# Kernel optimization log

Hardware: AMD Instinct MI355X
Metric: run time of the kernel (lower is better)

## Reference

```python
import jax, jax.numpy as jnp
import numpy as np

D_IN = 1024
D_OUT = 1024
N_HEADS = 16
HEAD_DIM = D_IN // N_HEADS      # 64
HEAD_DIM_V = D_OUT // N_HEADS   # 64


def setup_inputs() -> dict:
    key = jax.random.key(0)
    ks = jax.random.split(key, 7)
    s = 0.02
    x = jax.random.normal(ks[0], (4, 2048, D_IN), dtype=jnp.float32)
    Wq = jax.random.normal(ks[1], (D_IN, D_IN), dtype=jnp.float32) * s
    bq = jnp.zeros((D_IN,), dtype=jnp.float32)
    Wk = jax.random.normal(ks[2], (D_IN, D_IN), dtype=jnp.float32) * s
    bk = jnp.zeros((D_IN,), dtype=jnp.float32)
    Wv = jax.random.normal(ks[3], (D_IN, D_OUT), dtype=jnp.float32) * s
    bv = jnp.zeros((D_OUT,), dtype=jnp.float32)
    return {"x": x, "Wq": Wq, "bq": bq, "Wk": Wk, "bk": bk, "Wv": Wv, "bv": bv}


def reference(x, Wq, bq, Wk, bk, Wv, bv):
    B, S, _ = x.shape
    scale = jnp.sqrt(jnp.asarray(HEAD_DIM, dtype=jnp.float32))
    # projections -> [B, S, H, Dh] -> [B, H, S, Dh]
    q = (x @ Wq + bq).reshape(B, S, N_HEADS, HEAD_DIM).transpose(0, 2, 1, 3)
    k = (x @ Wk + bk).reshape(B, S, N_HEADS, HEAD_DIM).transpose(0, 2, 1, 3)
    v = (x @ Wv + bv).reshape(B, S, N_HEADS, HEAD_DIM_V).transpose(0, 2, 1, 3)
    # [B, H, S, S] attention scores (naive full materialization, as in source)
    scores = jnp.einsum("bhsd,bhtd->bhst", q, k) / scale
    weights = jax.nn.softmax(scores, axis=-1)
    out = jnp.einsum("bhst,bhtd->bhsd", weights, v)
    # [B, H, S, Dv] -> [B, S, H*Dv]  (out_projection NOT applied in source forward)
    return out.transpose(0, 2, 1, 3).reshape(B, S, N_HEADS * HEAD_DIM_V)
```

## Files before the change

### kernel.cpp

```cpp
#include <hip/hip_runtime.h>

#define B_  4
#define S_  2048
#define D_  1024
#define H_  16
#define DH_ 64
#define M_  (B_ * S_)

typedef __attribute__((ext_vector_type(8))) short short8;
typedef __attribute__((ext_vector_type(4))) float floatx4;

__device__ __forceinline__ float bf2f(unsigned short u) {
    union { unsigned int i; float f; } v; v.i = ((unsigned int)u) << 16; return v.f;
}
__device__ __forceinline__ unsigned short f2bf(float f) {
    union { float f; unsigned int i; } v; v.f = f;
    unsigned int r = v.i + 0x7fffu + ((v.i >> 16) & 1u);
    return (unsigned short)(r >> 16);
}
__device__ __forceinline__ unsigned int pk_trunc(float a, float b) {
#if __has_builtin(__builtin_amdgcn_perm)
    return __builtin_amdgcn_perm(__float_as_uint(b), __float_as_uint(a), 0x07060302u);
#else
    return (__float_as_uint(a) >> 16) | (__float_as_uint(b) & 0xffff0000u);
#endif
}

#if __has_builtin(__builtin_amdgcn_exp2f)
#define EXP2(x) __builtin_amdgcn_exp2f(x)
#else
#define EXP2(x) __expf(0.6931471805599453f * (x))
#endif

typedef const __attribute__((address_space(1))) unsigned int* gas_ptr;
typedef __attribute__((address_space(3))) unsigned int* las_ptr;
__device__ __forceinline__ void async_cp16(const void* g, void* l) {
    __builtin_amdgcn_global_load_lds((gas_ptr)g, (las_ptr)l, 16, 0, 0);
}

__global__ __launch_bounds__(256) void cast_x_kernel(
    const float* __restrict__ x, unsigned short* __restrict__ Ax)
{
    int i4 = blockIdx.x * 256 + threadIdx.x;
    float4 v = reinterpret_cast<const float4*>(x)[i4];
    ushort4 o;
    o.x = f2bf(v.x); o.y = f2bf(v.y); o.z = f2bf(v.z); o.w = f2bf(v.w);
    reinterpret_cast<ushort4*>(Ax)[i4] = o;
}

__global__ __launch_bounds__(256) void cast_w_T_kernel(
    const float* __restrict__ W0, const float* __restrict__ W1,
    const float* __restrict__ W2,
    unsigned short* __restrict__ T0, unsigned short* __restrict__ T1,
    unsigned short* __restrict__ T2)
{
    const float* W = blockIdx.z == 0 ? W0 : (blockIdx.z == 1 ? W1 : W2);
    unsigned short* Wt = blockIdx.z == 0 ? T0 : (blockIdx.z == 1 ? T1 : T2);

    __shared__ unsigned short T[64][72];
    const int t = threadIdx.x;
    const int k0 = blockIdx.x * 64, n0 = blockIdx.y * 64;

    #pragma unroll
    for (int p = 0; p < 4; ++p) {
        int kr = p * 16 + (t >> 4);
        int nc = (t & 15) * 4;
        float4 v = *reinterpret_cast<const float4*>(W + (size_t)(k0 + kr) * D_ + n0 + nc);
        T[nc + 0][kr] = f2bf(v.x);
        T[nc + 1][kr] = f2bf(v.y);
        T[nc + 2][kr] = f2bf(v.z);
        T[nc + 3][kr] = f2bf(v.w);
    }
    __syncthreads();

    const int nl = t >> 2, kc = (t & 3) * 16;
    size_t base = (size_t)(n0 + nl) * D_ + k0 + kc;
    *reinterpret_cast<short8*>(Wt + base)     = *reinterpret_cast<const short8*>(&T[nl][kc]);
    *reinterpret_cast<short8*>(Wt + base + 8) = *reinterpret_cast<const short8*>(&T[nl][kc + 8]);
}

__global__ __launch_bounds__(256) void gemm_qkv_mfma(
    const unsigned short* __restrict__ Ax,
    const unsigned short* __restrict__ Wtq,
    const unsigned short* __restrict__ Wtk,
    const unsigned short* __restrict__ Wtv,
    const float* __restrict__ bq, const float* __restrict__ bk,
    const float* __restrict__ bv,
    unsigned short* __restrict__ Q, unsigned short* __restrict__ K,
    unsigned short* __restrict__ Vtg)
{
    __shared__ unsigned short As[128 * 64];
    __shared__ unsigned short Bs[128 * 64];

    const int tid = threadIdx.x;
    const int lane = tid & 63;
    const int w = tid >> 6;
    const int wm = (w >> 1) * 64, wn = (w & 1) * 64;
    const int l15 = lane & 15, quad = lane >> 4;

    const int hw   = blockIdx.x;
    const int xcd  = hw & 7;
    const int slot = hw >> 3;
    const int gcol = slot >> 3;
    const int mi   = slot & 7;
    const int m0   = (xcd * 8 + mi) * 128;
    const int n0   = (gcol & 7) * 128;
    const int mat  = gcol >> 3;

    const unsigned short* Wt = mat == 0 ? Wtq : (mat == 1 ? Wtk : Wtv);
    const float* bias        = mat == 0 ? bq  : (mat == 1 ? bk  : bv);

    const int arow = tid >> 3;
    const int acol = (tid & 7) * 8;

    floatx4 acc[4][4] = {};

    for (int kb = 0; kb < 16; ++kb) {
        int cb = kb * 64;
        __syncthreads();
        #pragma unroll
        for (int r = 0; r < 4; ++r) {
            async_cp16(Ax + (size_t)(m0 + r * 32 + arow) * D_ + cb + acol,
                       As + (r * 32 + arow) * 64 + acol);
            async_cp16(Wt + (size_t)(n0 + r * 32 + arow) * D_ + cb + acol,
                       Bs + (r * 32 + arow) * 64 + acol);
        }
        __syncthreads();

        #pragma unroll
        for (int kk = 0; kk < 2; ++kk) {
            short8 af[4], bf[4];
            #pragma unroll
            for (int i = 0; i < 4; ++i)
                af[i] = *reinterpret_cast<const short8*>(As + (wm + i * 16 + l15) * 64 + kk * 32 + quad * 8);
            #pragma unroll
            for (int j = 0; j < 4; ++j)
                bf[j] = *reinterpret_cast<const short8*>(Bs + (wn + j * 16 + l15) * 64 + kk * 32 + quad * 8);
            #pragma unroll
            for (int i = 0; i < 4; ++i)
                #pragma unroll
                for (int j = 0; j < 4; ++j)
                    acc[i][j] = __builtin_amdgcn_mfma_f32_16x16x32_bf16(af[i], bf[j], acc[i][j], 0, 0, 0);
        }
    }

    float bb[4];
    #pragma unroll
    for (int j = 0; j < 4; ++j) bb[j] = bias[n0 + wn + j * 16 + l15];

    if (mat == 2) {
        const int b = m0 >> 11;
        #pragma unroll
        for (int i = 0; i < 4; ++i) {
            int srow = (m0 & 2047) + wm + i * 16 + quad * 4;
            #pragma unroll
            for (int j = 0; j < 4; ++j) {
                int col = n0 + wn + j * 16 + l15;
                ushort4 o;
                o.x = f2bf(acc[i][j][0] + bb[j]);
                o.y = f2bf(acc[i][j][1] + bb[j]);
                o.z = f2bf(acc[i][j][2] + bb[j]);
                o.w = f2bf(acc[i][j][3] + bb[j]);
                *reinterpret_cast<ushort4*>(Vtg + (size_t)(b * 1024 + col) * S_ + srow) = o;
            }
        }
    } else {
        unsigned short* C = (mat == 0) ? Q : K;
        const float sc = (mat == 0) ? 0.18033688011112042f : 1.0f;
        #pragma unroll
        for (int i = 0; i < 4; ++i)
            #pragma unroll
            for (int r = 0; r < 4; ++r) {
                int row = m0 + wm + i * 16 + quad * 4 + r;
                #pragma unroll
                for (int j = 0; j < 4; ++j)
                    C[(size_t)row * D_ + n0 + wn + j * 16 + l15] = f2bf((acc[i][j][r] + bb[j]) * sc);
            }
    }
}

#define KT_   64
#define PITCH 72

__global__ __launch_bounds__(256, 4) void attn_mfma(
    const unsigned short* __restrict__ Qg,
    const unsigned short* __restrict__ Kg,
    const unsigned short* __restrict__ Vtg,
    float* __restrict__ out)
{
    __shared__ unsigned short Ks[KT_ * PITCH];
    __shared__ unsigned short Vt[DH_ * PITCH];

    const int tid  = threadIdx.x;
    const int wq   = tid >> 6;
    const int lane = tid & 63;
    const int l15  = lane & 15;
    const int quad = lane >> 4;

    const int id  = blockIdx.x;
    const int bh  = (id & 7) * 8 + ((id >> 3) & 7);
    const int qt  = id >> 6;
    const int b   = bh >> 4;
    const int colbase = (bh & 15) * DH_;
    const int rowQ0 = b * S_ + qt * 128;

    short8 qf[2][2];
    #pragma unroll
    for (int g = 0; g < 2; ++g) {
        int qrow = rowQ0 + wq * 32 + g * 16 + l15;
        qf[g][0] = *reinterpret_cast<const short8*>(Qg + (size_t)qrow * D_ + colbase + quad * 8);
        qf[g][1] = *reinterpret_cast<const short8*>(Qg + (size_t)qrow * D_ + colbase + 32 + quad * 8);
    }

    short8 vones;
    #pragma unroll
    for (int i = 0; i < 8; ++i) vones[i] = (short)0x3F80;

    floatx4 Oacc[2][4] = {};
    floatx4 Lacc[2] = {};

    const int srow = tid >> 3;
    const int sc8  = (tid & 7) * 8;
    const int vc  = sc8 >> 4;
    const int vqk = (sc8 >> 2) & 3;
    const int vk0 = ((vc & 1) << 2) + ((vc >> 1) << 5) + (vqk << 3);

    const unsigned short* Kbase = Kg + (size_t)(b * S_) * D_ + colbase;
    const unsigned short* Vbase = Vtg + (size_t)(bh * 64) * S_;

    short8 kpre[2], vpre[2];
    #pragma unroll
    for (int p = 0; p < 2; ++p) {
        kpre[p] = *reinterpret_cast<const short8*>(Kbase + (size_t)(p * 32 + srow) * D_ + sc8);
        vpre[p] = *reinterpret_cast<const short8*>(Vbase + (size_t)(p * 32 + srow) * S_ + sc8);
    }

    for (int kt = 0; kt < S_ / KT_; ++kt) {
        __syncthreads();
        #pragma unroll
        for (int p = 0; p < 2; ++p) {
            *reinterpret_cast<short8*>(&Ks[(p * 32 + srow) * PITCH + sc8]) = kpre[p];
            uint4 u = __builtin_bit_cast(uint4, vpre[p]);
            uint2 lo, hi;
            lo.x = u.x; lo.y = u.y; hi.x = u.z; hi.y = u.w;
            *reinterpret_cast<uint2*>(&Vt[(p * 32 + srow) * PITCH + vk0])     = lo;
            *reinterpret_cast<uint2*>(&Vt[(p * 32 + srow) * PITCH + vk0 + 8]) = hi;
        }
        if (kt + 1 < S_ / KT_) {
            int off = (kt + 1) * KT_;
            #pragma unroll
            for (int p = 0; p < 2; ++p) {
                kpre[p] = *reinterpret_cast<const short8*>(Kbase + (size_t)(off + p * 32 + srow) * D_ + sc8);
                vpre[p] = *reinterpret_cast<const short8*>(Vbase + (size_t)(p * 32 + srow) * S_ + off + sc8);
            }
        }
        __syncthreads();

        #pragma unroll
        for (int half = 0; half < 2; ++half) {
            floatx4 s_[2][2];
            #pragma unroll
            for (int ci = 0; ci < 2; ++ci) {
                int c = half * 2 + ci;
                short8 kf0 = *reinterpret_cast<const short8*>(&Ks[(c * 16 + l15) * PITCH + quad * 8]);
                short8 kf1 = *reinterpret_cast<const short8*>(&Ks[(c * 16 + l15) * PITCH + 32 + quad * 8]);
                #pragma unroll
                for (int g = 0; g < 2; ++g) {
                    floatx4 a = {0.f, 0.f, 0.f, 0.f};
                    a = __builtin_amdgcn_mfma_f32_16x16x32_bf16(kf0, qf[g][0], a, 0, 0, 0);
                    a = __builtin_amdgcn_mfma_f32_16x16x32_bf16(kf1, qf[g][1], a, 0, 0, 0);
                    s_[g][ci] = a;
                }
            }
            short8 pa[2];
            #pragma unroll
            for (int g = 0; g < 2; ++g) {
                float p00 = EXP2(s_[g][0][0]), p01 = EXP2(s_[g][0][1]);
                float p02 = EXP2(s_[g][0][2]), p03 = EXP2(s_[g][0][3]);
                float p10 = EXP2(s_[g][1][0]), p11 = EXP2(s_[g][1][1]);
                float p12 = EXP2(s_[g][1][2]), p13 = EXP2(s_[g][1][3]);
                uint4 pu;
                pu.x = pk_trunc(p00, p01);
                pu.y = pk_trunc(p02, p03);
                pu.z = pk_trunc(p10, p11);
                pu.w = pk_trunc(p12, p13);
                pa[g] = __builtin_bit_cast(short8, pu);
            }
            #pragma unroll
            for (int g = 0; g < 2; ++g)
                Lacc[g] = __builtin_amdgcn_mfma_f32_16x16x32_bf16(pa[g], vones, Lacc[g], 0, 0, 0);
            #pragma unroll
            for (int d = 0; d < 4; ++d) {
                short8 vf = *reinterpret_cast<const short8*>(
                    &Vt[(d * 16 + l15) * PITCH + half * 32 + quad * 8]);
                #pragma unroll
                for (int g = 0; g < 2; ++g)
                    Oacc[g][d] = __builtin_amdgcn_mfma_f32_16x16x32_bf16(pa[g], vf, Oacc[g][d], 0, 0, 0);
            }
        }
    }

    #pragma unroll
    for (int g = 0; g < 2; ++g) {
        int orow = rowQ0 + wq * 32 + g * 16 + quad * 4;
        #pragma unroll
        for (int r = 0; r < 4; ++r) {
            float inv = 1.f / Lacc[g][r];
            #pragma unroll
            for (int d = 0; d < 4; ++d)
                out[(size_t)(orow + r) * D_ + colbase + d * 16 + l15] = Oacc[g][d][r] * inv;
        }
    }
}

extern "C" void kernel_launch(void* const* d_in, const int* in_sizes, int n_in,
                              void* d_out, int out_size, void* d_ws, size_t ws_size,
                              hipStream_t stream) {
    const float* x  = (const float*)d_in[0];
    const float* Wq = (const float*)d_in[1];
    const float* bq = (const float*)d_in[2];
    const float* Wk = (const float*)d_in[3];
    const float* bk = (const float*)d_in[4];
    const float* Wv = (const float*)d_in[5];
    const float* bv = (const float*)d_in[6];
    float* out = (float*)d_out;

    unsigned short* Q   = (unsigned short*)d_ws;
    unsigned short* K   = Q + (size_t)M_ * D_;
    unsigned short* Vtg = K + (size_t)M_ * D_;
    unsigned short* Ax  = Vtg + (size_t)M_ * D_;
    unsigned short* Wtq = Ax + (size_t)M_ * D_;
    unsigned short* Wtk = Wtq + (size_t)D_ * D_;
    unsigned short* Wtv = Wtk + (size_t)D_ * D_;

    cast_x_kernel<<<M_ * D_ / 4 / 256, 256, 0, stream>>>(x, Ax);
    dim3 gw(16, 16, 3);
    cast_w_T_kernel<<<gw, 256, 0, stream>>>(Wq, Wk, Wv, Wtq, Wtk, Wtv);

    gemm_qkv_mfma<<<1536, 256, 0, stream>>>(Ax, Wtq, Wtk, Wtv, bq, bk, bv, Q, K, Vtg);

    attn_mfma<<<1024, 256, 0, stream>>>(Q, K, Vtg, out);
}
```

Baseline: 246.0 us.

## Rewrite QKV GEMM as 256x256-tile, 8-wave, multi-stage async-pipelined kernel

Replaces the 128x128 single-buffered QKV projection GEMM with a 256x256 tile per 512-thread block. It uses a three-stage async global-to-LDS pipeline with explicit vmcnt waits, an XOR-swizzled LDS layout, and interleaved barriers with setprio around the MFMA bursts. The goal is to hide global load latency, cut LDS bank conflicts and raise operand reuse per tile. In exchange it uses 128 KB of LDS, which allows one block per CU. The grid shrinks to 384 blocks, so the GEMM may suffer tail and occupancy effects.

```diff
diff --git a/kernel.cpp b/kernel.cpp
--- a/kernel.cpp
+++ b/kernel.cpp
@@ -37,6 +37,9 @@
 __device__ __forceinline__ void async_cp16(const void* g, void* l) {
     __builtin_amdgcn_global_load_lds((gas_ptr)g, (las_ptr)l, 16, 0, 0);
 }
+
+#define VMC4 asm volatile("s_waitcnt vmcnt(4)" ::: "memory")
+#define VMC0 asm volatile("s_waitcnt vmcnt(0)" ::: "memory")
 
 __global__ __launch_bounds__(256) void cast_x_kernel(
     const float* __restrict__ x, unsigned short* __restrict__ Ax)
@@ -79,7 +82,7 @@
     *reinterpret_cast<short8*>(Wt + base + 8) = *reinterpret_cast<const short8*>(&T[nl][kc + 8]);
 }
 
-__global__ __launch_bounds__(256) void gemm_qkv_mfma(
+__global__ __launch_bounds__(512) void gemm_qkv_mfma(
     const unsigned short* __restrict__ Ax,
     const unsigned short* __restrict__ Wtq,
     const unsigned short* __restrict__ Wtk,
@@ -89,92 +92,127 @@
     unsigned short* __restrict__ Q, unsigned short* __restrict__ K,
     unsigned short* __restrict__ Vtg)
 {
-    __shared__ unsigned short As[128 * 64];
-    __shared__ unsigned short Bs[128 * 64];
-
-    const int tid = threadIdx.x;
+    __shared__ unsigned short lds[65536];
+
+    const int tid  = threadIdx.x;
     const int lane = tid & 63;
-    const int w = tid >> 6;
-    const int wm = (w >> 1) * 64, wn = (w & 1) * 64;
-    const int l15 = lane & 15, quad = lane >> 4;
-
-    const int hw   = blockIdx.x;
-    const int xcd  = hw & 7;
-    const int slot = hw >> 3;
-    const int gcol = slot >> 3;
-    const int mi   = slot & 7;
-    const int m0   = (xcd * 8 + mi) * 128;
-    const int n0   = (gcol & 7) * 128;
-    const int mat  = gcol >> 3;
-
-    const unsigned short* Wt = mat == 0 ? Wtq : (mat == 1 ? Wtk : Wtv);
-    const float* bias        = mat == 0 ? bq  : (mat == 1 ? bk  : bv);
-
-    const int arow = tid >> 3;
-    const int acol = (tid & 7) * 8;
-
-    floatx4 acc[4][4] = {};
-
-    for (int kb = 0; kb < 16; ++kb) {
-        int cb = kb * 64;
-        __syncthreads();
-        #pragma unroll
-        for (int r = 0; r < 4; ++r) {
-            async_cp16(Ax + (size_t)(m0 + r * 32 + arow) * D_ + cb + acol,
-                       As + (r * 32 + arow) * 64 + acol);
-            async_cp16(Wt + (size_t)(n0 + r * 32 + arow) * D_ + cb + acol,
-                       Bs + (r * 32 + arow) * 64 + acol);
-        }
-        __syncthreads();
-
-        #pragma unroll
-        for (int kk = 0; kk < 2; ++kk) {
-            short8 af[4], bf[4];
-            #pragma unroll
-            for (int i = 0; i < 4; ++i)
-                af[i] = *reinterpret_cast<const short8*>(As + (wm + i * 16 + l15) * 64 + kk * 32 + quad * 8);
-            #pragma unroll
-            for (int j = 0; j < 4; ++j)
-                bf[j] = *reinterpret_cast<const short8*>(Bs + (wn + j * 16 + l15) * 64 + kk * 32 + quad * 8);
-            #pragma unroll
-            for (int i = 0; i < 4; ++i)
+    const int w    = tid >> 6;
+    const int wm   = w >> 2;
+    const int wn   = w & 3;
+    const int l15  = lane & 15, quad = lane >> 4;
+
+    const int pl   = tid >> 3;
+    const int sl   = tid & 7;
+    const int xx   = sl ^ (pl & 7);
+    const int sro  = pl * 2 + (xx >> 2);
+    const int sc   = (xx & 3) * 8;
+    const int ldst = tid * 8;
+
+    const int fb = (l15 >> 1) * 64 + (((((l15 & 1) << 2) | quad)) ^ (l15 >> 1)) * 8;
+
+    const int id  = blockIdx.x;
+    const int wg  = (id & 7) * 48 + (id >> 3);
+    const int nb  = wg >> 5;
+    const int mb  = wg & 31;
+    const int m0  = mb * 256;
+    const int N0  = nb * 256;
+    const int mat = N0 >> 10;
+    const int n0m = N0 & 1023;
+
+    const unsigned short* Wtb = mat == 0 ? Wtq : (mat == 1 ? Wtk : Wtv);
+    const float* bias         = mat == 0 ? bq  : (mat == 1 ? bk  : bv);
+
+    #define STG(G, rowbase, kcol, reg) do { \
+        async_cp16((G) + (size_t)((rowbase) + sro) * 1024 + (kcol) + sc,       lds + (reg) + ldst); \
+        async_cp16((G) + (size_t)((rowbase) + 128 + sro) * 1024 + (kcol) + sc, lds + (reg) + 4096 + ldst); \
+    } while (0)
+
+    floatx4 acc[8][4] = {};
+    short8 bfr[4];
+
+    STG(Ax,  m0,  0,  0);
+    STG(Wtb, n0m, 0,  16384);
+    STG(Ax,  m0,  32, 8192);
+    STG(Wtb, n0m, 32, 24576);
+    STG(Ax,  m0,  64, 32768);
+    STG(Wtb, n0m, 64, 49152);
+    VMC4;
+    __builtin_amdgcn_s_barrier();
+
+    #define PH(bufS, ksub, mh, STAGE_STMT, WAIT_STMT) do { \
+        short8 af[4]; \
+        _Pragma("unroll") \
+        for (int i = 0; i < 4; ++i) \
+            af[i] = *reinterpret_cast<const short8*>(lds + (bufS) + (ksub) * 8192 + wm * 4096 + ((mh) * 4 + i) * 512 + fb); \
+        if ((mh) == 0) { \
+            _Pragma("unroll") \
+            for (int j = 0; j < 4; ++j) \
+                bfr[j] = *reinterpret_cast<const short8*>(lds + (bufS) + 16384 + (ksub) * 8192 + wn * 2048 + j * 512 + fb); \
+        } \
+        STAGE_STMT; \
+        __builtin_amdgcn_s_barrier(); \
+        asm volatile("s_waitcnt lgkmcnt(0)" ::: "memory"); \
+        __builtin_amdgcn_sched_barrier(0); \
+        __builtin_amdgcn_s_setprio(1); \
+        _Pragma("unroll") \
+        for (int i = 0; i < 4; ++i) \
+            _Pragma("unroll") \
+            for (int j = 0; j < 4; ++j) \
+                acc[(mh) * 4 + i][j] = __builtin_amdgcn_mfma_f32_16x16x32_bf16(af[i], bfr[j], acc[(mh) * 4 + i][j], 0, 0, 0); \
+        __builtin_amdgcn_s_setprio(0); \
+        WAIT_STMT; \
+        __builtin_amdgcn_s_barrier(); \
+    } while (0)
+
+    #pragma unroll 1
+    for (int it = 0; it < 8; ++it) {
+        const int  t1 = 2 * it + 1;
+        const bool nl = (it < 7);
+        const int  kA = t1 * 64;
+        const int  kB = kA + 64;
+        const int  kC = kA + 128;
+        PH(0,     0, 0, STG(Ax,  m0,  kA + 32, 40960), );
+        PH(0,     0, 1, STG(Wtb, n0m, kA + 32, 57344), );
+        PH(0,     1, 0, if (nl) STG(Ax,  m0,  kB, 0), );
+        PH(0,     1, 1, if (nl) STG(Wtb, n0m, kB, 16384), { if (nl) VMC4; else VMC0; });
+        PH(32768, 0, 0, if (nl) STG(Ax,  m0,  kB + 32, 8192), );
+        PH(32768, 0, 1, if (nl) STG(Wtb, n0m, kB + 32, 24576), );
+        PH(32768, 1, 0, if (nl) STG(Ax,  m0,  kC, 32768), );
+        PH(32768, 1, 1, if (nl) STG(Wtb, n0m, kC, 49152), { if (nl) VMC4; });
+    }
+
+    float bb[4];
+    #pragma unroll
+    for (int j = 0; j < 4; ++j) bb[j] = bias[n0m + wn * 64 + j * 16 + l15];
+
+    if (mat == 2) {
+        const int bI    = m0 >> 11;
+        const int sbase = (m0 & 2047) + wm * 128;
+        #pragma unroll
+        for (int mf = 0; mf < 8; ++mf) {
+            int srow = sbase + mf * 16 + quad * 4;
+            #pragma unroll
+            for (int j = 0; j < 4; ++j) {
+                int col = n0m + wn * 64 + j * 16 + l15;
+                ushort4 o;
+                o.x = f2bf(acc[mf][j][0] + bb[j]);
+                o.y = f2bf(acc[mf][j][1] + bb[j]);
+                o.z = f2bf(acc[mf][j][2] + bb[j]);
+                o.w = f2bf(acc[mf][j][3] + bb[j]);
+                *reinterpret_cast<ushort4*>(Vtg + (size_t)(bI * 1024 + col) * S_ + srow) = o;
+            }
+        }
+    } else {
+        unsigned short* C = (mat == 0) ? Q : K;
+        const float scq = (mat == 0) ? 0.18033688011112042f : 1.0f;
+        #pragma unroll
+        for (int mf = 0; mf < 8; ++mf)
+            #pragma unroll
+            for (int r = 0; r < 4; ++r) {
+                int row = m0 + wm * 128 + mf * 16 + quad * 4 + r;
                 #pragma unroll
                 for (int j = 0; j < 4; ++j)
-                    acc[i][j] = __builtin_amdgcn_mfma_f32_16x16x32_bf16(af[i], bf[j], acc[i][j], 0, 0, 0);
-        }
-    }
-
-    float bb[4];
-    #pragma unroll
-    for (int j = 0; j < 4; ++j) bb[j] = bias[n0 + wn + j * 16 + l15];
-
-    if (mat == 2) {
-        const int b = m0 >> 11;
-        #pragma unroll
-        for (int i = 0; i < 4; ++i) {
-            int srow = (m0 & 2047) + wm + i * 16 + quad * 4;
-            #pragma unroll
-            for (int j = 0; j < 4; ++j) {
-                int col = n0 + wn + j * 16 + l15;
-                ushort4 o;
-                o.x = f2bf(acc[i][j][0] + bb[j]);
-                o.y = f2bf(acc[i][j][1] + bb[j]);
-                o.z = f2bf(acc[i][j][2] + bb[j]);
-                o.w = f2bf(acc[i][j][3] + bb[j]);
-                *reinterpret_cast<ushort4*>(Vtg + (size_t)(b * 1024 + col) * S_ + srow) = o;
-            }
-        }
-    } else {
-        unsigned short* C = (mat == 0) ? Q : K;
-        const float sc = (mat == 0) ? 0.18033688011112042f : 1.0f;
-        #pragma unroll
-        for (int i = 0; i < 4; ++i)
-            #pragma unroll
-            for (int r = 0; r < 4; ++r) {
-                int row = m0 + wm + i * 16 + quad * 4 + r;
-                #pragma unroll
-                for (int j = 0; j < 4; ++j)
-                    C[(size_t)row * D_ + n0 + wn + j * 16 + l15] = f2bf((acc[i][j][r] + bb[j]) * sc);
+                    C[(size_t)row * D_ + n0m + wn * 64 + j * 16 + l15] = f2bf((acc[mf][j][r] + bb[j]) * scq);
             }
     }
 }
@@ -337,7 +375,7 @@
     dim3 gw(16, 16, 3);
     cast_w_T_kernel<<<gw, 256, 0, stream>>>(Wq, Wk, Wv, Wtq, Wtk, Wtv);
 
-    gemm_qkv_mfma<<<1536, 256, 0, stream>>>(Ax, Wtq, Wtk, Wtv, bq, bk, bv, Q, K, Vtg);
+    gemm_qkv_mfma<<<384, 512, 0, stream>>>(Ax, Wtq, Wtk, Wtv, bq, bk, bv, Q, K, Vtg);
 
     attn_mfma<<<1024, 256, 0, stream>>>(Q, K, Vtg, out);
 }
```

After: 243.6 us. About the same (-1.0%).
